# Kernel optimization log

Measured on AMD Instinct MI355X. Metric: run time of the kernel, lower is better.

Reference implementation:

```python
import jax, jax.numpy as jnp
import numpy as np

H = 16        # num_attention_heads
E = 1024      # hidden_size
D = E // H    # attention_head_size = 64
M = 1024      # max_position_embeddings
EPS = 1e-12


def setup_inputs() -> dict:
    key = jax.random.key(0)
    ks = jax.random.split(key, 12)
    s = 0.02
    B, S = 8, 1024
    return {
        "hidden_states": jax.random.normal(ks[0], (B, S, E), jnp.float32),
        "Wq": jax.random.normal(ks[1], (E, E), jnp.float32) * s,
        "bq": jnp.zeros((E,), jnp.float32),
        "Wk": jax.random.normal(ks[2], (E, E), jnp.float32) * s,
        "bk": jnp.zeros((E,), jnp.float32),
        "Wv": jax.random.normal(ks[3], (E, E), jnp.float32) * s,
        "bv": jnp.zeros((E,), jnp.float32),
        "dist_emb": jax.random.normal(ks[4], (2 * M - 1, D), jnp.float32) * s,
        "Wo": jax.random.normal(ks[5], (E, E), jnp.float32) * s,
        "bo": jnp.zeros((E,), jnp.float32),
        "ln_gamma": jnp.ones((E,), jnp.float32),
        "ln_beta": jnp.zeros((E,), jnp.float32),
    }


def reference(hidden_states, Wq, bq, Wk, bk, Wv, bv, dist_emb, Wo, bo, ln_gamma, ln_beta):
    B, S, _ = hidden_states.shape

    def heads(x):  # [B,S,E] -> [B,H,S,D]
        return x.reshape(B, S, H, D).transpose(0, 2, 1, 3)

    q = heads(hidden_states @ Wq + bq)
    k = heads(hidden_states @ Wk + bk)
    v = heads(hidden_states @ Wv + bv)

    scores = jnp.einsum("bhqd,bhkd->bhqk", q, k)

    # relative_key_query positional bias
    pos_l = jnp.arange(S)[:, None]
    pos_r = jnp.arange(S)[None, :]
    dist_idx = pos_l - pos_r + M - 1            # [S,S] in [0, 2M-2]
    pos_emb = dist_emb[dist_idx]                # [S,S,D]  (l, r, d)
    rel_q = jnp.einsum("bhld,lrd->bhlr", q, pos_emb)
    rel_k = jnp.einsum("bhrd,lrd->bhlr", k, pos_emb)
    scores = (scores + rel_q + rel_k) / jnp.sqrt(jnp.asarray(D, scores.dtype))

    probs = jax.nn.softmax(scores, axis=-1)     # dropout prob = 0 (eval)
    ctx = jnp.einsum("bhqk,bhkd->bhqd", probs, v)
    ctx = ctx.transpose(0, 2, 1, 3).reshape(B, S, E)

    # BertSelfOutput: dense + residual + LayerNorm
    h = ctx @ Wo + bo + hidden_states
    mu = jnp.mean(h, axis=-1, keepdims=True)
    var = jnp.mean(jnp.square(h - mu), axis=-1, keepdims=True)
    out = (h - mu) * jax.lax.rsqrt(var + EPS) * ln_gamma + ln_beta
    return out
```

## Files before the change

kernel.cpp:

```cpp
#include <hip/hip_runtime.h>


typedef unsigned short u16;
typedef unsigned int u32;
typedef unsigned long long u64;
typedef __bf16 bf16x8 __attribute__((ext_vector_type(8)));
typedef float  f32x4  __attribute__((ext_vector_type(4)));
typedef int    i32x4  __attribute__((ext_vector_type(4)));

__device__ __forceinline__ float b2f(u16 u) {
  union { u32 i; float f; } x;
  x.i = ((u32)u) << 16;
  return x.f;
}
__device__ __forceinline__ u16 f2b_manual(float f) {
  union { float f; u32 u; } x;
  x.f = f;
  return (u16)((x.u + 0x7FFFu + ((x.u >> 16) & 1u)) >> 16);
}
#if __has_builtin(__builtin_amdgcn_cvt_pk_bf16_f32)
typedef __bf16 bf16x2 __attribute__((ext_vector_type(2)));
__device__ __forceinline__ u32 cvt2(float a, float b) {
  union { bf16x2 v; u32 u; } x;
  x.v = __builtin_amdgcn_cvt_pk_bf16_f32(a, b);
  return x.u;
}
#else
__device__ __forceinline__ u32 cvt2(float a, float b) {
  return (u32)f2b_manual(a) | ((u32)f2b_manual(b) << 16);
}
#endif
__device__ __forceinline__ u16 f2b(float f) { return (u16)(cvt2(f, f) & 0xffffu); }

union LdU { i32x4 i4; bf16x8 b8; };
__device__ __forceinline__ bf16x8 ldb8(const u16* p) {
  LdU u; u.i4 = *(const i32x4*)p; return u.b8;
}
__device__ __forceinline__ void pack8(u16* dst, const float* src) {
  f32x4 lo = *(const f32x4*)src, hi = *(const f32x4*)(src + 4);
  i32x4 v;
  v.x = (int)cvt2(lo.x, lo.y); v.y = (int)cvt2(lo.z, lo.w);
  v.z = (int)cvt2(hi.x, hi.y); v.w = (int)cvt2(hi.z, hi.w);
  *(i32x4*)dst = v;
}
#define MFMA16(a, b, c) __builtin_amdgcn_mfma_f32_16x16x32_bf16((a), (b), (c), 0, 0, 0)

template <int C>
__device__ __forceinline__ float dppmov(float x) {
  union { float f; int i; } a, r;
  a.f = x;
  r.i = __builtin_amdgcn_update_dpp(0, a.i, C, 0xF, 0xF, true);
  return r.f;
}
__device__ __forceinline__ float rsum16(float x) {
  x += dppmov<0xB1>(x);
  x += dppmov<0x4E>(x);
  x += dppmov<0x141>(x);
  x += dppmov<0x140>(x);
  return x;
}
__device__ __forceinline__ float fexp2(float x) {
#if __has_builtin(__builtin_amdgcn_exp2f)
  return __builtin_amdgcn_exp2f(x);
#else
  return exp2f(x);
#endif
}

#if __has_builtin(__builtin_amdgcn_global_load_lds)
#define HAS_GLDS 1
typedef __attribute__((address_space(3))) u32 as3_u32;
typedef const __attribute__((address_space(1))) u32 as1_u32;
__device__ __forceinline__ void gld16(const u16* g, u16* lds_wave_base) {
  __builtin_amdgcn_global_load_lds(
      (as1_u32*)g, (as3_u32*)(u32)(u64)lds_wave_base, 16, 0, 0);
}
#else
#define HAS_GLDS 0
__device__ __forceinline__ void gld16_fb(const u16* g, u16* lds_wave_base,
                                         int lane) {
  *(i32x4*)(lds_wave_base + lane * 8) = *(const i32x4*)g;
}
#endif

#define SQRT_C2 0.42466090f

__global__ __launch_bounds__(256) void convX(
    const float* __restrict__ X, u16* __restrict__ Xb) {
  int i = (blockIdx.x * 256 + threadIdx.x) * 8;
  pack8(&Xb[i], &X[i]);
}

__global__ __launch_bounds__(256) void convD(
    const float* __restrict__ dist, u16* __restrict__ distb) {
  int i = (blockIdx.x * 256 + threadIdx.x) * 8;
  if (i < 2047 * 64) {
    float t[8];
#pragma unroll
    for (int j = 0; j < 8; j++) t[j] = dist[i + j] * SQRT_C2;
    pack8(&distb[i], t);
  }
}

__global__ __launch_bounds__(256) void convWt4(
    const float* __restrict__ W0, const float* __restrict__ W1,
    const float* __restrict__ W2, const float* __restrict__ W3,
    u16* __restrict__ Wt) {
  __shared__ float tile[64][65];
  const int tid = threadIdx.x;
  const int k0 = blockIdx.x * 64, m0 = blockIdx.y * 64;
  const int z = blockIdx.z;
  const float* W = (z == 0) ? W0 : (z == 1) ? W1 : (z == 2) ? W2 : W3;
  u16* Wtz = Wt + (size_t)z * 1024 * 1024;
#pragma unroll
  for (int it = 0; it < 4; it++) {
    int row = (tid >> 4) + 16 * it;
    int col = (tid & 15) * 4;
    f32x4 v = *(const f32x4*)&W[(size_t)(k0 + row) * 1024 + m0 + col];
    tile[row][col] = v.x; tile[row][col + 1] = v.y;
    tile[row][col + 2] = v.z; tile[row][col + 3] = v.w;
  }
  __syncthreads();
#pragma unroll
  for (int it = 0; it < 4; it++) {
    int mr = (tid >> 4) + 16 * it;
    int kc = (tid & 15) * 4;
    u32 w0 = cvt2(tile[kc][mr], tile[kc + 1][mr]);
    u32 w1 = cvt2(tile[kc + 2][mr], tile[kc + 3][mr]);
    *(u64*)&Wtz[(size_t)(m0 + mr) * 1024 + k0 + kc] = (u64)w0 | ((u64)w1 << 32);
  }
}

__global__ __launch_bounds__(256) void transV(
    const u16* __restrict__ V, u16* __restrict__ Vt) {
  __shared__ u16 tile[64][72];
  const int tid = threadIdx.x;
  const int bh = blockIdx.y, b = bh >> 4, h = bh & 15;
  const int s0 = blockIdx.x << 6;
  const u16* Vb = V + (size_t)(b * 1024) * 1024 + h * 64;
  {
    int rp = tid >> 3, a = tid & 7;
    const u16* src = &Vb[(size_t)(s0 + 2 * rp) * 1024 + a * 8];
    i32x4 va = *(const i32x4*)src;
    i32x4 vb2 = *(const i32x4*)(src + 1024);
    u16 ta[8] __attribute__((aligned(16)));
    u16 tb[8] __attribute__((aligned(16)));
    *(i32x4*)ta = va; *(i32x4*)tb = vb2;
    int colb = ((((rp >> 2) ^ a) << 3) | ((2 * rp) & 7));
#pragma unroll
    for (int j = 0; j < 8; j++)
      *(u32*)&tile[a * 8 + j][colb] = (u32)ta[j] | ((u32)tb[j] << 16);
  }
  __syncthreads();
  int d = tid >> 2, cc = tid & 3;
  int sw = (d >> 3) & 7;
  i32x4 lo = *(const i32x4*)&tile[d][((2 * cc) ^ sw) << 3];
  i32x4 hi = *(const i32x4*)&tile[d][((2 * cc + 1) ^ sw) << 3];
  u16* dst = Vt + ((size_t)bh * 64 + d) * 1024 + s0 + cc * 16;
  *(i32x4*)dst = lo;
  *(i32x4*)(dst + 8) = hi;
}

template <int RESID, int OUTF32, int QKV>
__global__ __launch_bounds__(256) void gemm_bb(
    const u16* __restrict__ A, const u16* __restrict__ Wt,
    const float* __restrict__ bias, const float* __restrict__ biasK,
    const float* __restrict__ biasV, const float* __restrict__ resid,
    float* __restrict__ outF, u16* __restrict__ outB, int N, int K, int M) {
  __shared__ u16 sA[128 * 64];
  __shared__ u16 sW[128 * 64];

  const int tid = threadIdx.x;
  const int lane = tid & 63, w = tid >> 6;
  const int quad = lane >> 4, lb = lane & 15;
  const int m0 = blockIdx.y * 128, n0 = blockIdx.x * 128;

  const int srow = lane >> 3;
  const int gcol = ((lane & 7) ^ srow) << 3;

  f32x4 acc[2][8] = {};

  for (int k0 = 0; k0 < K; k0 += 64) {
#pragma unroll
    for (int j = 0; j < 4; j++) {
      int rb = (4 * w + j) * 8;
      const u16* ga = &A[(size_t)(n0 + rb + srow) * K + k0 + gcol];
      const u16* gw = &Wt[(size_t)(m0 + rb + srow) * K + k0 + gcol];
#if HAS_GLDS
      gld16(ga, &sA[rb * 64]);
      gld16(gw, &sW[rb * 64]);
#else
      gld16_fb(ga, &sA[rb * 64], lane);
      gld16_fb(gw, &sW[rb * 64], lane);
#endif
    }
    __syncthreads();

    const int r0 = 32 * w + lb;
    const int sw0 = r0 & 7;
    bf16x8 a00 = ldb8(&sA[r0 * 64 + ((quad ^ sw0) << 3)]);
    bf16x8 a01 = ldb8(&sA[r0 * 64 + (((4 + quad) ^ sw0) << 3)]);
    bf16x8 a10 = ldb8(&sA[(r0 + 16) * 64 + ((quad ^ sw0) << 3)]);
    bf16x8 a11 = ldb8(&sA[(r0 + 16) * 64 + (((4 + quad) ^ sw0) << 3)]);
#pragma unroll
    for (int t = 0; t < 8; t++) {
      int n = 16 * t + lb;
      int swn = n & 7;
      bf16x8 b0 = ldb8(&sW[n * 64 + ((quad ^ swn) << 3)]);
      bf16x8 b1 = ldb8(&sW[n * 64 + (((4 + quad) ^ swn) << 3)]);
      acc[0][t] = MFMA16(a00, b0, acc[0][t]);
      acc[0][t] = MFMA16(a01, b1, acc[0][t]);
      acc[1][t] = MFMA16(a10, b0, acc[1][t]);
      acc[1][t] = MFMA16(a11, b1, acc[1][t]);
    }
    __syncthreads();
  }

  const float* bp = bias;
  u16* outSeg = outB;
  float osc = 1.0f;
  int mbase = m0;
  if (QKV) {
    int seg = m0 >> 10;
    bp = (seg == 0) ? bias : (seg == 1) ? biasK : biasV;
    outSeg = outB + (size_t)seg * ((size_t)8192 * 1024);
    osc = (seg < 2) ? SQRT_C2 : 1.0f;
    mbase = m0 & 1023;
  }

#pragma unroll
  for (int half = 0; half < 2; half++)
#pragma unroll
    for (int t = 0; t < 8; t++) {
      int colw = mbase + 16 * t + lb;
      float bv = bp[colw];
#pragma unroll
      for (int i = 0; i < 4; i++) {
        int rowg = n0 + 32 * w + 16 * half + quad * 4 + i;
        float v = acc[half][t][i] + bv;
        if (RESID) v += resid[(size_t)rowg * M + colw];
        if (QKV) v *= osc;
        if (OUTF32) outF[(size_t)rowg * M + colw] = v;
        else        outSeg[(size_t)rowg * (QKV ? 1024 : M) + colw] = f2b(v);
      }
    }
}

__global__ __launch_bounds__(256) void attn(
    const u16* __restrict__ Q, const u16* __restrict__ Kv,
    const u16* __restrict__ Vt, const u16* __restrict__ distb,
    u16* __restrict__ ctx) {
  __shared__ u16 sK[64][72];
  __shared__ u16 sVt[64 * 64];
  __shared__ u16 sP[128 * 64];
  __shared__ u16 sGq[80 * 64];
  __shared__ u16 sGk[80 * 64];

  const int tid = threadIdx.x;
  const int lane = tid & 63, w = tid >> 6;
  const int quad = lane >> 4, lb = lane & 15;
  const int f = blockIdx.y * 16 + blockIdx.x;
  const int xcd = f & 7, slot = f >> 3;
  const int bh = (xcd << 4) | (slot & 15);
  const int q0 = (slot >> 4) << 6;
  const int b = bh >> 4, h = bh & 15;
  const int S = 1024, E = 1024;
  const u16* Qb = Q  + (size_t)(b * S) * E + h * 64;
  const u16* Kb = Kv + (size_t)(b * S) * E + h * 64;
  const u16* Vtb = Vt + (size_t)bh * 64 * 1024;

  const int sr = tid >> 3, g8 = tid & 7, sc8 = g8 << 3;
  const int vswz = (g8 ^ (sr & 7)) << 3;

  {
    u16(*sQ)[72] = (u16(*)[72])sGk;
    *(i32x4*)&sQ[sr][sc8] = *(const i32x4*)&Qb[(size_t)(q0 + sr) * E + sc8];
    *(i32x4*)&sQ[sr + 32][sc8] =
        *(const i32x4*)&Qb[(size_t)(q0 + sr + 32) * E + sc8];
    *(i32x4*)&sK[sr][sc8] = *(const i32x4*)&Kb[(size_t)sr * E + sc8];
    *(i32x4*)&sK[sr + 32][sc8] =
        *(const i32x4*)&Kb[(size_t)(sr + 32) * E + sc8];
    *(i32x4*)&sVt[sr * 64 + vswz] = *(const i32x4*)&Vtb[(size_t)sr * 1024 + sc8];
    *(i32x4*)&sVt[(sr + 32) * 64 + vswz] =
        *(const i32x4*)&Vtb[(size_t)(sr + 32) * 1024 + sc8];
    const int dbase = q0 + 960;
#pragma unroll
    for (int j = 0; j < 4; j++) {
      int p = sr + 32 * j;
      int g = dbase + p;
      if (g > 2046) g = 2046;
      *(i32x4*)&sP[p * 64 + vswz] = *(const i32x4*)&distb[(size_t)g * 64 + sc8];
    }
  }
  __syncthreads();

  const int row = 16 * w + lb;
  bf16x8 aq0, aq1;
  {
    u16(*sQ)[72] = (u16(*)[72])sGk;
    aq0 = ldb8(&sQ[row][quad * 8]);
    aq1 = ldb8(&sQ[row][32 + quad * 8]);
  }

  const int lsw = (lb & 7) << 3;
  const u16* kb   = &sK[lb][quad * 8];
  const u16* vbp0 = &sVt[lb * 64 + ((quad ^ (lb & 7)) << 3)];
  const u16* vbp1 = &sVt[lb * 64 + (((4 + quad) ^ (lb & 7)) << 3)];
  const u16* akb = &sK[row][quad * 8];
  const u16* pb0 = &sP[lb * 64 + ((quad ^ (lb & 7)) << 3)];
  const u16* pb1 = &sP[lb * 64 + (((4 + quad) ^ (lb & 7)) << 3)];
  const int cswz = (16 * w + 4 * quad) ^ lsw;
  u16* gqsb = sGq + (lb * 64 + cswz - 1024 * w);
  u16* gksb = sGk + (lb * 64 + cswz + 1024 * w - 3072);
  u16* psb  = &sK[16 * w + 4 * quad][lb];
  const int rl_ = 16 * w + 4 * quad;
  const u16* gqa_[4];
  const u16* gka_[4][4];
#pragma unroll
  for (int i = 0; i < 4; i++) {
    int rl = rl_ + i;
    int c3 = rl - lb + 15;
    int sw8 = (c3 & 7) << 3;
    gqa_[i] = &sGq[((c3 - 16 * w) << 6) + (rl ^ sw8)];
    int pk = rl - lb + 15;
#pragma unroll
    for (int t = 0; t < 4; t++)
      gka_[i][t] = &sGk[(pk << 6) + ((16 * t + lb) ^ sw8)];
  }
  const u16* kg0 = Kb + (size_t)(64 + sr) * E + sc8;
  const u16* kg1 = kg0 + (size_t)32 * E;
  const u16* vg0 = Vtb + (size_t)sr * 1024 + 64 + sc8;
  const u16* vg1 = vg0 + (size_t)32 * 1024;
  const u16* dg0 = distb + (size_t)(q0 - 64 + 960 + sr) * 64 + sc8;
  const u16* dg1 = dg0 + (size_t)32 * 64;
  u16* wk0 = &sK[sr][sc8];        u16* wk1 = &sK[sr + 32][sc8];
  u16* wv0 = &sVt[sr * 64 + vswz]; u16* wv1 = wv0 + 2048;
  u16* wp0 = &sP[sr * 64 + vswz];  u16* wp1 = wp0 + 2048;

  const int uqlo = w, uqhi = w + 4;
  const int uklo = 3 - w, ukhi = 7 - w;

  f32x4 accO[4] = {};
  float l_i[4] = {0.f, 0.f, 0.f, 0.f};

  for (int kt = 0; kt < 16; kt++) {
    const int xorv = (kt & 1) << 6;

    i32x4 kr0, kr1, vr0, vr1, dr0, dr1;
    if (kt < 15) {
      kr0 = *(const i32x4*)kg0;
      kr1 = *(const i32x4*)kg1;
      vr0 = *(const i32x4*)vg0;
      vr1 = *(const i32x4*)vg1;
      dr0 = *(const i32x4*)dg0;
      dr1 = *(const i32x4*)dg1;
    }

    __builtin_amdgcn_s_setprio(1);
    f32x4 accS[4] = {};
#pragma unroll
    for (int t = 0; t < 4; t++) {
      bf16x8 b0 = ldb8(kb + 1152 * t);
      bf16x8 b1 = ldb8(kb + 1152 * t + 32);
      accS[t] = MFMA16(aq0, b0, accS[t]);
      accS[t] = MFMA16(aq1, b1, accS[t]);
    }
    bf16x8 ak0 = ldb8(akb);
    bf16x8 ak1 = ldb8(akb + 32);
    const u16* pA0 = pb0 + (xorv ? 4096 : 0);
    const u16* pA1 = pb1 + (xorv ? 4096 : 0);
    const u16* pB0 = pb0 + (xorv ? -4096 : 0);
    const u16* pB1 = pb1 + (xorv ? -4096 : 0);
#pragma unroll
    for (int u = 0; u < 8; u++) {
      const bool doq = (u >= uqlo) && (u <= uqhi);
      const bool dok = (u >= uklo) && (u <= ukhi);
      if (doq || dok) {
        bf16x8 p0 = ldb8((u < 4 ? pA0 : pB0) + 1024 * u);
        bf16x8 p1 = ldb8((u < 4 ? pA1 : pB1) + 1024 * u);
        if (doq) {
          f32x4 gq = {};
          gq = MFMA16(aq0, p0, gq);
          gq = MFMA16(aq1, p1, gq);
          *(u32*)(gqsb + 1024 * u) = cvt2(gq[0], gq[1]);
          *(u32*)(gqsb + 1024 * u + 2) = cvt2(gq[2], gq[3]);
        }
        if (dok) {
          f32x4 gk = {};
          gk = MFMA16(ak0, p0, gk);
          gk = MFMA16(ak1, p1, gk);
          *(u32*)(gksb + 1024 * u) = cvt2(gk[0], gk[1]);
          *(u32*)(gksb + 1024 * u + 2) = cvt2(gk[2], gk[3]);
        }
      }
    }
    __builtin_amdgcn_s_setprio(0);
    __syncthreads();

    float pr[4][4];
#pragma unroll
    for (int t = 0; t < 4; t++) {
#pragma unroll
      for (int i = 0; i < 4; i++) {
        float s = accS[t][i] + b2f(gqa_[i][1024 * (3 - t)]) +
                  b2f(*gka_[i][t]);
        float e = fexp2(s);
        pr[t][i] = e;
        l_i[i] += e;
      }
    }

#pragma unroll
    for (int t = 0; t < 4; t++)
#pragma unroll
      for (int i = 0; i < 4; i++)
        psb[72 * i + 16 * t] = f2b(pr[t][i]);

    bf16x8 ap0 = ldb8(akb);
    bf16x8 ap1 = ldb8(akb + 32);
    __builtin_amdgcn_s_setprio(1);
#pragma unroll
    for (int t = 0; t < 4; t++) {
      bf16x8 v0 = ldb8(vbp0 + 1024 * t);
      bf16x8 v1 = ldb8(vbp1 + 1024 * t);
      accO[t] = MFMA16(ap0, v0, accO[t]);
      accO[t] = MFMA16(ap1, v1, accO[t]);
    }
    __builtin_amdgcn_s_setprio(0);
    __syncthreads();

    if (kt < 15) {
      const int pxn = ((kt + 1) & 1) ? 4096 : 0;
      *(i32x4*)wk0 = kr0;
      *(i32x4*)wk1 = kr1;
      *(i32x4*)wv0 = vr0;
      *(i32x4*)wv1 = vr1;
      *(i32x4*)(wp0 + pxn) = dr0;
      *(i32x4*)(wp1 + pxn) = dr1;
      kg0 += (size_t)64 * E; kg1 += (size_t)64 * E;
      vg0 += 64;             vg1 += 64;
      dg0 -= 64 * 64;        dg1 -= 64 * 64;
      __syncthreads();
    }
  }

#pragma unroll
  for (int i = 0; i < 4; i++) l_i[i] = rsum16(l_i[i]);

  u16* Cb = ctx + (size_t)(b * S) * E + h * 64;
#pragma unroll
  for (int t = 0; t < 4; t++)
#pragma unroll
    for (int i = 0; i < 4; i++) {
      int rl = 16 * w + quad * 4 + i;
      Cb[(size_t)(q0 + rl) * E + 16 * t + lb] = f2b(accO[t][i] / l_i[i]);
    }
}

__global__ __launch_bounds__(256) void lnorm(
    const float* __restrict__ Hp, const float* __restrict__ gamma,
    const float* __restrict__ beta, float* __restrict__ out) {
  __shared__ float red[8];
  const int rowb = blockIdx.x, tid = threadIdx.x;
  const float* hr = Hp + (size_t)rowb * 1024;
  f32x4 v = *(const f32x4*)&hr[tid * 4];
  float s = v.x + v.y + v.z + v.w;
  float q = v.x * v.x + v.y * v.y + v.z * v.z + v.w * v.w;
#pragma unroll
  for (int d = 1; d < 64; d <<= 1) {
    s += __shfl_xor(s, d, 64);
    q += __shfl_xor(q, d, 64);
  }
  int w = tid >> 6, lane = tid & 63;
  if (lane == 0) { red[w] = s; red[4 + w] = q; }
  __syncthreads();
  s = red[0] + red[1] + red[2] + red[3];
  q = red[4] + red[5] + red[6] + red[7];
  float mu = s * (1.f / 1024.f);
  float var = q * (1.f / 1024.f) - mu * mu;
  float rstd = rsqrtf(var + 1e-12f);
  float* orow = out + (size_t)rowb * 1024;
  f32x4 o;
#pragma unroll
  for (int j = 0; j < 4; j++) {
    int c = tid * 4 + j;
    o[j] = (v[j] - mu) * rstd * gamma[c] + beta[c];
  }
  *(f32x4*)&orow[tid * 4] = o;
}

extern "C" void kernel_launch(void* const* d_in, const int* in_sizes, int n_in,
                              void* d_out, int out_size, void* d_ws,
                              size_t ws_size, hipStream_t stream) {
  const float* X    = (const float*)d_in[0];
  const float* Wq   = (const float*)d_in[1];
  const float* bq   = (const float*)d_in[2];
  const float* Wk   = (const float*)d_in[3];
  const float* bk   = (const float*)d_in[4];
  const float* Wv   = (const float*)d_in[5];
  const float* bv   = (const float*)d_in[6];
  const float* dist = (const float*)d_in[7];
  const float* Wo   = (const float*)d_in[8];
  const float* bo   = (const float*)d_in[9];
  const float* gam  = (const float*)d_in[10];
  const float* bet  = (const float*)d_in[11];

  const size_t NE = (size_t)8192 * 1024;
  char* ws = (char*)d_ws;
  u16* Qw = (u16*)(ws);
  u16* Kw = (u16*)(ws + 2 * NE);
  u16* Vw = (u16*)(ws + 4 * NE);
  u16* Cw = (u16*)(ws + 6 * NE);
  float* Hp = (float*)ws;

  char* ob = (char*)d_out;
  u16* Wt4 = (u16*)(ob);
  u16* Wto = (u16*)(ob + (6u << 20));
  u16* Xb  = (u16*)(ob + (8u << 20));
  u16* Vtg = (u16*)(ob + (8u << 20));
  u16* distb = (u16*)(ob + (26u << 20));

  dim3 bb(256);
  convWt4<<<dim3(16, 16, 4), bb, 0, stream>>>(Wq, Wk, Wv, Wo, Wt4);
  convX<<<dim3(4096), bb, 0, stream>>>(X, Xb);
  convD<<<dim3(64), bb, 0, stream>>>(dist, distb);

  gemm_bb<0, 0, 1><<<dim3(64, 24), bb, 0, stream>>>(
      Xb, Wt4, bq, bk, bv, nullptr, nullptr, Qw, 8192, 1024, 3072);
  transV<<<dim3(16, 128), bb, 0, stream>>>(Vw, Vtg);
  attn<<<dim3(16, 128), bb, 0, stream>>>(Qw, Kw, Vtg, distb, Cw);
  gemm_bb<1, 1, 0><<<dim3(64, 8), bb, 0, stream>>>(
      Cw, Wto, bo, nullptr, nullptr, X, Hp, nullptr, 8192, 1024, 1024);
  lnorm<<<dim3(8192), bb, 0, stream>>>(Hp, gam, bet, (float*)d_out);
}
```

Baseline: 409.0 us.

## Double-buffer K/V tiles in attention to drop one barrier per iteration

The attention kernel's K and V^T shared-memory tiles become double-buffered. The next tile's prefetched registers are stored into the alternate buffer right after the first barrier, so the trailing store-and-sync phase is removed and each iteration runs with two barriers instead of three. This uses more LDS per block (an extra 64x72 and 64x64 bf16 buffer), which could reduce occupancy. The P tile that aliases sK now also alternates buffers. Note that sQ aliases sGk and the initial V fill goes to buffer 0.

```diff
diff --git a/kernel.cpp b/kernel.cpp
--- a/kernel.cpp
+++ b/kernel.cpp
@@ -250,8 +250,8 @@
     const u16* __restrict__ Q, const u16* __restrict__ Kv,
     const u16* __restrict__ Vt, const u16* __restrict__ distb,
     u16* __restrict__ ctx) {
-  __shared__ u16 sK[64][72];
-  __shared__ u16 sVt[64 * 64];
+  __shared__ u16 sK[2][64][72];
+  __shared__ u16 sVt[2 * 64 * 64];
   __shared__ u16 sP[128 * 64];
   __shared__ u16 sGq[80 * 64];
   __shared__ u16 sGk[80 * 64];
@@ -277,8 +277,8 @@
     *(i32x4*)&sQ[sr][sc8] = *(const i32x4*)&Qb[(size_t)(q0 + sr) * E + sc8];
     *(i32x4*)&sQ[sr + 32][sc8] =
         *(const i32x4*)&Qb[(size_t)(q0 + sr + 32) * E + sc8];
-    *(i32x4*)&sK[sr][sc8] = *(const i32x4*)&Kb[(size_t)sr * E + sc8];
-    *(i32x4*)&sK[sr + 32][sc8] =
+    *(i32x4*)&sK[0][sr][sc8] = *(const i32x4*)&Kb[(size_t)sr * E + sc8];
+    *(i32x4*)&sK[0][sr + 32][sc8] =
         *(const i32x4*)&Kb[(size_t)(sr + 32) * E + sc8];
     *(i32x4*)&sVt[sr * 64 + vswz] = *(const i32x4*)&Vtb[(size_t)sr * 1024 + sc8];
     *(i32x4*)&sVt[(sr + 32) * 64 + vswz] =
@@ -303,16 +303,16 @@
   }
 
   const int lsw = (lb & 7) << 3;
-  const u16* kb   = &sK[lb][quad * 8];
-  const u16* vbp0 = &sVt[lb * 64 + ((quad ^ (lb & 7)) << 3)];
-  const u16* vbp1 = &sVt[lb * 64 + (((4 + quad) ^ (lb & 7)) << 3)];
-  const u16* akb = &sK[row][quad * 8];
+  const u16* kbB  = &sK[0][lb][quad * 8];
+  const u16* akbB = &sK[0][row][quad * 8];
+  u16* psbB       = &sK[0][16 * w + 4 * quad][lb];
+  const u16* vb0B = &sVt[lb * 64 + ((quad ^ (lb & 7)) << 3)];
+  const u16* vb1B = &sVt[lb * 64 + (((4 + quad) ^ (lb & 7)) << 3)];
   const u16* pb0 = &sP[lb * 64 + ((quad ^ (lb & 7)) << 3)];
   const u16* pb1 = &sP[lb * 64 + (((4 + quad) ^ (lb & 7)) << 3)];
   const int cswz = (16 * w + 4 * quad) ^ lsw;
   u16* gqsb = sGq + (lb * 64 + cswz - 1024 * w);
   u16* gksb = sGk + (lb * 64 + cswz + 1024 * w - 3072);
-  u16* psb  = &sK[16 * w + 4 * quad][lb];
   const int rl_ = 16 * w + 4 * quad;
   const u16* gqa_[4];
   const u16* gka_[4][4];
@@ -333,9 +333,10 @@
   const u16* vg1 = vg0 + (size_t)32 * 1024;
   const u16* dg0 = distb + (size_t)(q0 - 64 + 960 + sr) * 64 + sc8;
   const u16* dg1 = dg0 + (size_t)32 * 64;
-  u16* wk0 = &sK[sr][sc8];        u16* wk1 = &sK[sr + 32][sc8];
-  u16* wv0 = &sVt[sr * 64 + vswz]; u16* wv1 = wv0 + 2048;
-  u16* wp0 = &sP[sr * 64 + vswz];  u16* wp1 = wp0 + 2048;
+  u16* wk0B = &sK[0][sr][sc8];
+  u16* wk1B = &sK[0][sr + 32][sc8];
+  u16* wv0B = &sVt[sr * 64 + vswz];
+  u16* wp0  = &sP[sr * 64 + vswz];
 
   const int uqlo = w, uqhi = w + 4;
   const int uklo = 3 - w, ukhi = 7 - w;
@@ -344,7 +345,8 @@
   float l_i[4] = {0.f, 0.f, 0.f, 0.f};
 
   for (int kt = 0; kt < 16; kt++) {
-    const int xorv = (kt & 1) << 6;
+    const int cur = kt & 1, alt = cur ^ 1;
+    const int co = cur * 4608, vo = cur * 4096;
 
     i32x4 kr0, kr1, vr0, vr1, dr0, dr1;
     if (kt < 15) {
@@ -360,17 +362,17 @@
     f32x4 accS[4] = {};
 #pragma unroll
     for (int t = 0; t < 4; t++) {
-      bf16x8 b0 = ldb8(kb + 1152 * t);
-      bf16x8 b1 = ldb8(kb + 1152 * t + 32);
+      bf16x8 b0 = ldb8(kbB + co + 1152 * t);
+      bf16x8 b1 = ldb8(kbB + co + 1152 * t + 32);
       accS[t] = MFMA16(aq0, b0, accS[t]);
       accS[t] = MFMA16(aq1, b1, accS[t]);
     }
-    bf16x8 ak0 = ldb8(akb);
-    bf16x8 ak1 = ldb8(akb + 32);
-    const u16* pA0 = pb0 + (xorv ? 4096 : 0);
-    const u16* pA1 = pb1 + (xorv ? 4096 : 0);
-    const u16* pB0 = pb0 + (xorv ? -4096 : 0);
-    const u16* pB1 = pb1 + (xorv ? -4096 : 0);
+    bf16x8 ak0 = ldb8(akbB + co);
+    bf16x8 ak1 = ldb8(akbB + co + 32);
+    const u16* pA0 = pb0 + (cur ? 4096 : 0);
+    const u16* pA1 = pb1 + (cur ? 4096 : 0);
+    const u16* pB0 = pb0 + (cur ? -4096 : 0);
+    const u16* pB1 = pb1 + (cur ? -4096 : 0);
 #pragma unroll
     for (int u = 0; u < 8; u++) {
       const bool doq = (u >= uqlo) && (u <= uqhi);
@@ -397,6 +399,20 @@
     __builtin_amdgcn_s_setprio(0);
     __syncthreads();
 
+    if (kt < 15) {
+      const int ca = alt * 4608, va = alt * 4096;
+      const int pxn = alt ? 4096 : 0;
+      *(i32x4*)(wk0B + ca) = kr0;
+      *(i32x4*)(wk1B + ca) = kr1;
+      *(i32x4*)(wv0B + va) = vr0;
+      *(i32x4*)(wv0B + va + 2048) = vr1;
+      *(i32x4*)(wp0 + pxn) = dr0;
+      *(i32x4*)(wp0 + pxn + 2048) = dr1;
+      kg0 += (size_t)64 * E; kg1 += (size_t)64 * E;
+      vg0 += 64;             vg1 += 64;
+      dg0 -= 64 * 64;        dg1 -= 64 * 64;
+    }
+
     float pr[4][4];
 #pragma unroll
     for (int t = 0; t < 4; t++) {
@@ -414,34 +430,20 @@
     for (int t = 0; t < 4; t++)
 #pragma unroll
       for (int i = 0; i < 4; i++)
-        psb[72 * i + 16 * t] = f2b(pr[t][i]);
-
-    bf16x8 ap0 = ldb8(akb);
-    bf16x8 ap1 = ldb8(akb + 32);
+        psbB[co + 72 * i + 16 * t] = f2b(pr[t][i]);
+
+    bf16x8 ap0 = ldb8(akbB + co);
+    bf16x8 ap1 = ldb8(akbB + co + 32);
     __builtin_amdgcn_s_setprio(1);
 #pragma unroll
     for (int t = 0; t < 4; t++) {
-      bf16x8 v0 = ldb8(vbp0 + 1024 * t);
-      bf16x8 v1 = ldb8(vbp1 + 1024 * t);
+      bf16x8 v0 = ldb8(vb0B + vo + 1024 * t);
+      bf16x8 v1 = ldb8(vb1B + vo + 1024 * t);
       accO[t] = MFMA16(ap0, v0, accO[t]);
       accO[t] = MFMA16(ap1, v1, accO[t]);
     }
     __builtin_amdgcn_s_setprio(0);
     __syncthreads();
-
-    if (kt < 15) {
-      const int pxn = ((kt + 1) & 1) ? 4096 : 0;
-      *(i32x4*)wk0 = kr0;
-      *(i32x4*)wk1 = kr1;
-      *(i32x4*)wv0 = vr0;
-      *(i32x4*)wv1 = vr1;
-      *(i32x4*)(wp0 + pxn) = dr0;
-      *(i32x4*)(wp1 + pxn) = dr1;
-      kg0 += (size_t)64 * E; kg1 += (size_t)64 * E;
-      vg0 += 64;             vg1 += 64;
-      dg0 -= 64 * 64;        dg1 -= 64 * 64;
-      __syncthreads();
-    }
   }
 
 #pragma unroll
```

Measured after the change: 407.4 us. About the same (-0.4%).
